# Kernel tuning notes

Measured on AMD Instinct MI355X. Metric: run time of the kernel, lower is better.

Reference implementation:

```python
import jax, jax.numpy as jnp
import numpy as np

B, T, I = 256, 2048, 128
H, L = 128, 2


def setup_inputs() -> dict:
    key = jax.random.key(0)
    ks = jax.random.split(key, 12)
    s_in = 1.0 / np.sqrt(I)
    s_h = 1.0 / np.sqrt(H)
    return {
        "x": jax.random.normal(ks[0], (B, T, I), jnp.float32),
        "Wz": jax.random.normal(ks[1], (L, I, H), jnp.float32) * s_in,
        "bz": jax.random.normal(ks[2], (L, H), jnp.float32) * s_in,
        "Uz": jax.random.normal(ks[3], (L, H, H), jnp.float32) * s_h,
        "Wr": jax.random.normal(ks[4], (L, I, H), jnp.float32) * s_in,
        "br": jax.random.normal(ks[5], (L, H), jnp.float32) * s_in,
        "Ur": jax.random.normal(ks[6], (L, H, H), jnp.float32) * s_h,
        "Wh": jax.random.normal(ks[7], (L, I, H), jnp.float32) * s_in,
        "bh": jax.random.normal(ks[8], (L, H), jnp.float32) * s_in,
        "Uh": jax.random.normal(ks[9], (L, H, H), jnp.float32) * s_h,
        "fc_w": jax.random.normal(ks[10], (H, 1), jnp.float32) * s_h,
        "fc_b": jax.random.normal(ks[11], (1,), jnp.float32) * s_h,
    }


def _gru_forward(x, Wz, bz, Uz, Wr, br, Ur, Wh, bh, Uh, fc_w, fc_b):
    nl = Wz.shape[0]
    batch = x.shape[0]
    hid = Uz.shape[-1]
    # Precompute layer-0 input projections for all timesteps: [T, B, H]
    pz0 = jnp.einsum('bti,ih->tbh', x, Wz[0]) + bz[0]
    pr0 = jnp.einsum('bti,ih->tbh', x, Wr[0]) + br[0]
    ph0 = jnp.einsum('bti,ih->tbh', x, Wh[0]) + bh[0]

    def step(h, proj_t):
        az0, ar0, ah0 = proj_t  # each [B, H]
        new_h = []
        prev = None
        for l in range(nl):
            if l == 0:
                az, ar, ah = az0, ar0, ah0
            else:
                az = prev @ Wz[l] + bz[l]
                ar = prev @ Wr[l] + br[l]
                ah = prev @ Wh[l] + bh[l]
            hl = h[l]
            z = jax.nn.sigmoid(az + hl @ Uz[l])
            r = jax.nn.sigmoid(ar + hl @ Ur[l])
            h_tilde = jnp.tanh(ah + (r * hl) @ Uh[l])
            hl = (1.0 - z) * hl + z * h_tilde
            new_h.append(hl)
            prev = hl
        return jnp.stack(new_h), None

    h0 = jnp.zeros((nl, batch, hid), x.dtype)
    h_final, _ = jax.lax.scan(step, h0, (pz0, pr0, ph0))
    return h_final[-1] @ fc_w + fc_b


def reference(x, Wz, bz, Uz, Wr, br, Ur, Wh, bh, Uh, fc_w, fc_b):
    return _gru_forward(x, Wz, bz, Uz, Wr, br, Ur, Wh, bh, Uh, fc_w, fc_b)
```

## Files before the change

kernel.cpp:

```cpp
#include <hip/hip_runtime.h>
#include <hip/hip_bf16.h>
#include <stdint.h>

#define T_STEPS 2048
#define BATCH   256
#define IDIM    128
#define HDIM    128

typedef __bf16 bf16x2 __attribute__((ext_vector_type(2)));

#if __has_builtin(__builtin_amdgcn_fdot2_f32_bf16)
#define HAVE_DOT2 1
#else
#define HAVE_DOT2 0
#endif

static __device__ __forceinline__ float d2(uint32_t a, uint32_t b, float c) {
#if HAVE_DOT2
  return __builtin_amdgcn_fdot2_f32_bf16(__builtin_bit_cast(bf16x2, a),
                                         __builtin_bit_cast(bf16x2, b), c, false);
#else
  float alo = __builtin_bit_cast(float, a << 16);
  float ahi = __builtin_bit_cast(float, a & 0xffff0000u);
  float blo = __builtin_bit_cast(float, b << 16);
  float bhi = __builtin_bit_cast(float, b & 0xffff0000u);
  return c + alo * blo + ahi * bhi;
#endif
}

static __device__ __forceinline__ uint32_t pack_bf16(float lo, float hi) {
  uint32_t a = (uint32_t)__builtin_bit_cast(unsigned short, __float2bfloat16(lo));
  uint32_t b = (uint32_t)__builtin_bit_cast(unsigned short, __float2bfloat16(hi));
  return a | (b << 16);
}

static __device__ __forceinline__ float sigmoidf_(float x) {
  return 1.f / (1.f + __expf(-x));
}
static __device__ __forceinline__ float tanhf_(float x) {
  return 1.f - 2.f / (1.f + __expf(2.f * x));
}

__global__ void pack_weights(const float* __restrict__ Wz, const float* __restrict__ Uz,
                             const float* __restrict__ Wr, const float* __restrict__ Ur,
                             const float* __restrict__ Wh, const float* __restrict__ Uh,
                             uint32_t* __restrict__ wpack) {
  int idx = blockIdx.x * blockDim.x + threadIdx.x;
  if (idx >= 12 * 4 * 128 * 16) return;
  int p = idx & 15;
  int j = (idx >> 4) & 127;
  int q = (idx >> 11) & 3;
  int m = idx >> 13;
  const float* src;
  switch (m) {
    case 0:  src = Wz;          break;
    case 1:  src = Wr;          break;
    case 2:  src = Wh;          break;
    case 3:  src = Uz;          break;
    case 4:  src = Ur;          break;
    case 5:  src = Uh;          break;
    case 6:  src = Uz + 16384;  break;
    case 7:  src = Ur + 16384;  break;
    case 8:  src = Wz + 16384;  break;
    case 9:  src = Wr + 16384;  break;
    case 10: src = Wh + 16384;  break;
    default: src = Uh + 16384;  break;
  }
  int i = q * 32 + p * 2;
  float lo = src[i * 128 + j];
  float hi = src[(i + 1) * 128 + j];
  wpack[idx] = pack_bf16(lo, hi);
}

#define QD(M)                                                          \
  {                                                                    \
    float a0 = 0.f, a1 = 0.f;                                          \
    a0 = d2(w[M][0].x, v0.x, a0); a0 = d2(w[M][0].y, v0.y, a0);        \
    a0 = d2(w[M][0].z, v0.z, a0); a0 = d2(w[M][0].w, v0.w, a0);        \
    a0 = d2(w[M][1].x, v1.x, a0); a0 = d2(w[M][1].y, v1.y, a0);        \
    a0 = d2(w[M][1].z, v1.z, a0); a0 = d2(w[M][1].w, v1.w, a0);        \
    a1 = d2(w[M][2].x, v2.x, a1); a1 = d2(w[M][2].y, v2.y, a1);        \
    a1 = d2(w[M][2].z, v2.z, a1); a1 = d2(w[M][2].w, v2.w, a1);        \
    a1 = d2(w[M][3].x, v3.x, a1); a1 = d2(w[M][3].y, v3.y, a1);        \
    a1 = d2(w[M][3].z, v3.z, a1); a1 = d2(w[M][3].w, v3.w, a1);        \
    part[(M * 4 + q) * 128 + j] = a0 + a1;                             \
  }

#define LOADV(VB)                                                      \
  const uint4* vp = (const uint4*)(VB);                                \
  uint4 v0 = vp[q * 4 + 0], v1 = vp[q * 4 + 1],                        \
        v2 = vp[q * 4 + 2], v3 = vp[q * 4 + 3];

#define PSUM(M)                                                        \
  ((part[(M * 4 + 0) * 128 + j2] + part[(M * 4 + 1) * 128 + j2]) +     \
   (part[(M * 4 + 2) * 128 + j2] + part[(M * 4 + 3) * 128 + j2]))

static __device__ __forceinline__ void pair_store(uint32_t* dst, int j2, float v) {
  uint32_t me = (uint32_t)__builtin_bit_cast(unsigned short, __float2bfloat16(v));
  uint32_t other = __shfl_xor((unsigned int)me, 1, 64);
  if ((j2 & 1) == 0) dst[j2 >> 1] = me | (other << 16);
}

__launch_bounds__(512, 2)
__global__ void gru_persist(const float* __restrict__ x,
                            const float* __restrict__ bz, const float* __restrict__ br,
                            const float* __restrict__ bh,
                            const float* __restrict__ fcw, const float* __restrict__ fcb,
                            const uint32_t* __restrict__ wpack,
                            float* __restrict__ out) {
  __shared__ float part[12 * 4 * 128];
  __shared__ float h0f[128], h1f[128], z0f[128], z1f[128];
  __shared__ uint32_t xbf[64], h0bf[64], h1bf[64], rh0bf[64], rh1bf[64];
  __shared__ float biasL[6 * 128];

  const int tid = threadIdx.x;
  const int j = tid & 127;
  const int q = tid >> 7;
  const int b = blockIdx.x;

  uint4 w[12][4];
  {
    const uint4* wp4 = (const uint4*)wpack;
#pragma unroll
    for (int m = 0; m < 12; ++m)
#pragma unroll
      for (int p = 0; p < 4; ++p)
        w[m][p] = wp4[((m * 4 + q) * 128 + j) * 4 + p];
  }

  if (tid < 128) {
    h0f[tid] = 0.f; h1f[tid] = 0.f;
    biasL[0 * 128 + tid] = bz[tid];
    biasL[1 * 128 + tid] = br[tid];
    biasL[2 * 128 + tid] = bh[tid];
    biasL[3 * 128 + tid] = bz[128 + tid];
    biasL[4 * 128 + tid] = br[128 + tid];
    biasL[5 * 128 + tid] = bh[128 + tid];
  }
  if (tid < 64) { h0bf[tid] = 0u; h1bf[tid] = 0u; }
  const float2* xrow = (const float2*)(x + (size_t)b * T_STEPS * IDIM);
  if (tid < 64) {
    float2 v = xrow[tid];
    xbf[tid] = pack_bf16(v.x, v.y);
  }
  __syncthreads();

  float2 xpre = make_float2(0.f, 0.f);
  for (int t = 0; t < T_STEPS; ++t) {
    if (tid < 64) {
      int tn = (t + 1 < T_STEPS) ? (t + 1) : t;
      xpre = xrow[tn * 64 + tid];
    }

    { LOADV(xbf);  QD(0); QD(1); QD(2); }
    { LOADV(h0bf); QD(3); QD(4); }
    { LOADV(h1bf); QD(6); QD(7); }
    __syncthreads();

    if (tid < 128) {
      const int j2 = tid;
      float az = biasL[0 * 128 + j2] + PSUM(0) + PSUM(3);
      float ar = biasL[1 * 128 + j2] + PSUM(1) + PSUM(4);
      float z = sigmoidf_(az);
      float r = sigmoidf_(ar);
      z0f[j2] = z;
      pair_store(rh0bf, j2, r * h0f[j2]);
    }
    __syncthreads();

    { LOADV(rh0bf); QD(5); }
    __syncthreads();

    if (tid < 128) {
      const int j2 = tid;
      float ah = biasL[2 * 128 + j2] + PSUM(2) + PSUM(5);
      float ht = tanhf_(ah);
      float z = z0f[j2];
      float hn = (1.f - z) * h0f[j2] + z * ht;
      h0f[j2] = hn;
      pair_store(h0bf, j2, hn);
    }
    __syncthreads();

    { LOADV(h0bf); QD(8); QD(9); QD(10); }
    __syncthreads();

    if (tid < 128) {
      const int j2 = tid;
      float az = biasL[3 * 128 + j2] + PSUM(8) + PSUM(6);
      float ar = biasL[4 * 128 + j2] + PSUM(9) + PSUM(7);
      float z = sigmoidf_(az);
      float r = sigmoidf_(ar);
      z1f[j2] = z;
      pair_store(rh1bf, j2, r * h1f[j2]);
    }
    __syncthreads();

    { LOADV(rh1bf); QD(11); }
    __syncthreads();

    if (tid < 128) {
      const int j2 = tid;
      float ah = biasL[5 * 128 + j2] + PSUM(10) + PSUM(11);
      float ht = tanhf_(ah);
      float z = z1f[j2];
      float hn = (1.f - z) * h1f[j2] + z * ht;
      h1f[j2] = hn;
      pair_store(h1bf, j2, hn);
    }
    if (tid < 64) xbf[tid] = pack_bf16(xpre.x, xpre.y);
    __syncthreads();
  }

  if (tid < 128) part[tid] = h1f[tid] * fcw[tid];
  __syncthreads();
  if (tid == 0) {
    float s = fcb[0];
#pragma unroll 8
    for (int i = 0; i < 128; ++i) s += part[i];
    out[b] = s;
  }
}

extern "C" void kernel_launch(void* const* d_in, const int* in_sizes, int n_in,
                              void* d_out, int out_size, void* d_ws, size_t ws_size,
                              hipStream_t stream) {
  const float* x   = (const float*)d_in[0];
  const float* Wz  = (const float*)d_in[1];
  const float* bz  = (const float*)d_in[2];
  const float* Uz  = (const float*)d_in[3];
  const float* Wr  = (const float*)d_in[4];
  const float* br  = (const float*)d_in[5];
  const float* Ur  = (const float*)d_in[6];
  const float* Wh  = (const float*)d_in[7];
  const float* bh  = (const float*)d_in[8];
  const float* Uh  = (const float*)d_in[9];
  const float* fcw = (const float*)d_in[10];
  const float* fcb = (const float*)d_in[11];
  uint32_t* wpack = (uint32_t*)d_ws;

  hipLaunchKernelGGL(pack_weights, dim3(384), dim3(256), 0, stream,
                     Wz, Uz, Wr, Ur, Wh, Uh, wpack);
  hipLaunchKernelGGL(gru_persist, dim3(BATCH), dim3(512), 0, stream,
                     x, bz, br, bh, fcw, fcb, wpack, (float*)d_out);
}
```

Baseline: 5.260 ms.

## Precompute layer-0 input projections in a separate kernel before the recurrent loop

Adds an xproj kernel that computes the layer-0 input projections (x·W plus bias) for all timesteps up front and stores them in workspace as fp32, or as bf16 when workspace is short. The persistent GRU kernel then streams these precomputed values instead of doing three 128x128 matvecs per step, so it holds 9 weight matrices in registers instead of 12. It also spreads the gate activations over 256 threads and pins the weight registers with empty asm. The cost is an extra kernel and a large workspace round-trip, about 800MB in fp32, with a fallback to the old path when workspace is too small.

```diff
diff --git a/kernel.cpp b/kernel.cpp
--- a/kernel.cpp
+++ b/kernel.cpp
@@ -33,12 +33,245 @@
   uint32_t b = (uint32_t)__builtin_bit_cast(unsigned short, __float2bfloat16(hi));
   return a | (b << 16);
 }
-
+static __device__ __forceinline__ unsigned short bf16bits(float v) {
+  return __builtin_bit_cast(unsigned short, __float2bfloat16(v));
+}
 static __device__ __forceinline__ float sigmoidf_(float x) {
   return 1.f / (1.f + __expf(-x));
 }
 static __device__ __forceinline__ float tanhf_(float x) {
   return 1.f - 2.f / (1.f + __expf(2.f * x));
+}
+
+#define NWU (9 * 4 * 128 * 16)
+#define NWP (384 * 64)
+
+__global__ void pack2(const float* __restrict__ Wz, const float* __restrict__ Uz,
+                      const float* __restrict__ Wr, const float* __restrict__ Ur,
+                      const float* __restrict__ Wh, const float* __restrict__ Uh,
+                      uint32_t* __restrict__ wpackU, uint32_t* __restrict__ wpackP) {
+  int idx = blockIdx.x * blockDim.x + threadIdx.x;
+  if (idx < NWU) {
+    int p = idx & 15;
+    int j = (idx >> 4) & 127;
+    int q = (idx >> 11) & 3;
+    int m = idx >> 13;
+    const float* src;
+    switch (m) {
+      case 0:  src = Uz;          break;
+      case 1:  src = Ur;          break;
+      case 2:  src = Uh;          break;
+      case 3:  src = Wz + 16384;  break;
+      case 4:  src = Wr + 16384;  break;
+      case 5:  src = Wh + 16384;  break;
+      case 6:  src = Uz + 16384;  break;
+      case 7:  src = Ur + 16384;  break;
+      default: src = Uh + 16384;  break;
+    }
+    int i = q * 32 + p * 2;
+    wpackU[idx] = pack_bf16(src[i * 128 + j], src[(i + 1) * 128 + j]);
+  } else if (idx < NWU + NWP) {
+    int k = idx - NWU;
+    int p = k & 63;
+    int c = k >> 6;
+    int g = c >> 7;
+    int j = c & 127;
+    const float* src = (g == 0) ? Wz : (g == 1) ? Wr : Wh;
+    wpackP[k] = pack_bf16(src[2 * p * 128 + j], src[(2 * p + 1) * 128 + j]);
+  }
+}
+
+template <int MODE>
+__global__ void xproj(const float* __restrict__ x,
+                      const float* __restrict__ bz, const float* __restrict__ br,
+                      const float* __restrict__ bh,
+                      const uint32_t* __restrict__ wpackP, void* __restrict__ proj) {
+  __shared__ uint32_t xs[64];
+  const int c = threadIdx.x;
+  const int g = c >> 7;
+  const int j = c & 127;
+  uint32_t wc[64];
+#pragma unroll
+  for (int p = 0; p < 64; ++p) wc[p] = wpackP[c * 64 + p];
+  const float bias = ((g == 0) ? bz : (g == 1) ? br : bh)[j];
+
+  const long r0 = (long)blockIdx.x * 512;
+  for (int rr = 0; rr < 512; ++rr) {
+    const long r = r0 + rr;
+    if (c < 64) {
+      float2 v = ((const float2*)(x + r * 128))[c];
+      xs[c] = pack_bf16(v.x, v.y);
+    }
+    __syncthreads();
+    float acc = bias;
+#pragma unroll
+    for (int p = 0; p < 64; ++p) acc = d2(wc[p], xs[p], acc);
+    if (MODE == 0)
+      ((float*)proj)[r * 384 + c] = acc;
+    else
+      ((unsigned short*)proj)[r * 384 + c] = bf16bits(acc);
+    __syncthreads();
+  }
+}
+
+#define QD(M)                                                          \
+  {                                                                    \
+    float a0 = 0.f, a1 = 0.f;                                          \
+    a0 = d2(w[M][0].x, v0.x, a0); a0 = d2(w[M][0].y, v0.y, a0);        \
+    a0 = d2(w[M][0].z, v0.z, a0); a0 = d2(w[M][0].w, v0.w, a0);        \
+    a0 = d2(w[M][1].x, v1.x, a0); a0 = d2(w[M][1].y, v1.y, a0);        \
+    a0 = d2(w[M][1].z, v1.z, a0); a0 = d2(w[M][1].w, v1.w, a0);        \
+    a1 = d2(w[M][2].x, v2.x, a1); a1 = d2(w[M][2].y, v2.y, a1);        \
+    a1 = d2(w[M][2].z, v2.z, a1); a1 = d2(w[M][2].w, v2.w, a1);        \
+    a1 = d2(w[M][3].x, v3.x, a1); a1 = d2(w[M][3].y, v3.y, a1);        \
+    a1 = d2(w[M][3].z, v3.z, a1); a1 = d2(w[M][3].w, v3.w, a1);        \
+    part[(M * 4 + q) * 128 + j] = a0 + a1;                             \
+  }
+
+#define LOADV(VB)                                                      \
+  const uint4* vp = (const uint4*)(VB);                                \
+  uint4 v0 = vp[q * 4 + 0], v1 = vp[q * 4 + 1],                        \
+        v2 = vp[q * 4 + 2], v3 = vp[q * 4 + 3];
+
+#define PSUM(M)                                                        \
+  ((part[(M * 4 + 0) * 128 + j2] + part[(M * 4 + 1) * 128 + j2]) +     \
+   (part[(M * 4 + 2) * 128 + j2] + part[(M * 4 + 3) * 128 + j2]))
+
+template <int MODE>
+__launch_bounds__(512, 2)
+__global__ void gru_persist2(const void* __restrict__ proj,
+                             const float* __restrict__ bz1, const float* __restrict__ br1,
+                             const float* __restrict__ bh1,
+                             const float* __restrict__ fcw, const float* __restrict__ fcb,
+                             const uint32_t* __restrict__ wpackU,
+                             float* __restrict__ out) {
+  __shared__ float part[9 * 4 * 128];
+  __shared__ float h0f[128], h1f[128], z0f[128];
+  __shared__ __align__(16) uint32_t h0bf[64], h1bf[64], rh0bf[64], rh1bf[64];
+  __shared__ float pbuf[384];
+  __shared__ float biasL[3 * 128];
+
+  const int tid = threadIdx.x;
+  const int j = tid & 127;
+  const int q = tid >> 7;
+  const int b = blockIdx.x;
+
+  uint4 w[9][4];
+  {
+    const uint4* wp4 = (const uint4*)wpackU;
+#pragma unroll
+    for (int m = 0; m < 9; ++m)
+#pragma unroll
+      for (int p = 0; p < 4; ++p)
+        w[m][p] = wp4[((m * 4 + q) * 128 + j) * 4 + p];
+  }
+#pragma unroll
+  for (int m = 0; m < 9; ++m)
+#pragma unroll
+    for (int p = 0; p < 4; ++p)
+      asm volatile("" : "+v"(w[m][p].x), "+v"(w[m][p].y),
+                        "+v"(w[m][p].z), "+v"(w[m][p].w));
+
+  if (tid < 128) {
+    h0f[tid] = 0.f; h1f[tid] = 0.f;
+    biasL[0 * 128 + tid] = bz1[tid];
+    biasL[1 * 128 + tid] = br1[tid];
+    biasL[2 * 128 + tid] = bh1[tid];
+  }
+  if (tid < 64) { h0bf[tid] = 0u; h1bf[tid] = 0u; }
+
+  const float*    prow32 = (const float*)proj + (size_t)b * T_STEPS * 384;
+  const uint32_t* prow16 = (const uint32_t*)proj + (size_t)b * T_STEPS * 192;
+  float    pc32 = 0.f;
+  uint32_t pc16 = 0u;
+  if (MODE == 0) { if (tid < 384) pc32 = prow32[tid]; }
+  else           { if (tid < 192) pc16 = prow16[tid]; }
+  __syncthreads();
+
+  for (int t = 0; t < T_STEPS; ++t) {
+    float pn32 = 0.f; uint32_t pn16 = 0u;
+    {
+      const int tn = (t + 1 < T_STEPS) ? (t + 1) : t;
+      if (MODE == 0) { if (tid < 384) pn32 = prow32[(size_t)tn * 384 + tid]; }
+      else           { if (tid < 192) pn16 = prow16[(size_t)tn * 192 + tid]; }
+    }
+
+    { LOADV(h0bf); QD(0); QD(1); }
+    { LOADV(h1bf); QD(6); QD(7); }
+    if (MODE == 0) {
+      if (tid < 384) pbuf[tid] = pc32;
+    } else {
+      if (tid < 192) {
+        pbuf[2 * tid]     = __builtin_bit_cast(float, pc16 << 16);
+        pbuf[2 * tid + 1] = __builtin_bit_cast(float, pc16 & 0xffff0000u);
+      }
+    }
+    __syncthreads();
+
+    if (tid < 256) {
+      const int j2 = tid & 127;
+      const bool isz = tid < 128;
+      const int M = isz ? 0 : 1;
+      float a = pbuf[(isz ? 0 : 128) + j2] + PSUM(M);
+      float gv = sigmoidf_(a);
+      if (isz) z0f[j2] = gv;
+      else     ((unsigned short*)rh0bf)[j2] = bf16bits(gv * h0f[j2]);
+    }
+    __syncthreads();
+
+    { LOADV(rh0bf); QD(2); }
+    __syncthreads();
+
+    if (tid < 128) {
+      const int j2 = tid;
+      float a = pbuf[256 + j2] + PSUM(2);
+      float ht = tanhf_(a);
+      float h = h0f[j2];
+      float hn = fmaf(z0f[j2], ht - h, h);
+      h0f[j2] = hn;
+      ((unsigned short*)h0bf)[j2] = bf16bits(hn);
+    }
+    __syncthreads();
+
+    { LOADV(h0bf); QD(3); QD(4); QD(5); }
+    __syncthreads();
+
+    if (tid < 256) {
+      const int j2 = tid & 127;
+      const bool isz = tid < 128;
+      float a = isz ? (biasL[j2]       + PSUM(3) + PSUM(6))
+                    : (biasL[128 + j2] + PSUM(4) + PSUM(7));
+      float gv = sigmoidf_(a);
+      if (isz) z0f[j2] = gv;
+      else     ((unsigned short*)rh1bf)[j2] = bf16bits(gv * h1f[j2]);
+    }
+    __syncthreads();
+
+    { LOADV(rh1bf); QD(8); }
+    __syncthreads();
+
+    if (tid < 128) {
+      const int j2 = tid;
+      float a = biasL[256 + j2] + PSUM(5) + PSUM(8);
+      float ht = tanhf_(a);
+      float h = h1f[j2];
+      float hn = fmaf(z0f[j2], ht - h, h);
+      h1f[j2] = hn;
+      ((unsigned short*)h1bf)[j2] = bf16bits(hn);
+    }
+    __syncthreads();
+
+    pc32 = pn32; pc16 = pn16;
+  }
+
+  if (tid < 128) part[tid] = h1f[tid] * fcw[tid];
+  __syncthreads();
+  if (tid == 0) {
+    float s = fcb[0];
+#pragma unroll 8
+    for (int i = 0; i < 128; ++i) s += part[i];
+    out[b] = s;
+  }
 }
 
 __global__ void pack_weights(const float* __restrict__ Wz, const float* __restrict__ Uz,
@@ -67,36 +300,11 @@
     default: src = Uh + 16384;  break;
   }
   int i = q * 32 + p * 2;
-  float lo = src[i * 128 + j];
-  float hi = src[(i + 1) * 128 + j];
-  wpack[idx] = pack_bf16(lo, hi);
-}
-
-#define QD(M)                                                          \
-  {                                                                    \
-    float a0 = 0.f, a1 = 0.f;                                          \
-    a0 = d2(w[M][0].x, v0.x, a0); a0 = d2(w[M][0].y, v0.y, a0);        \
-    a0 = d2(w[M][0].z, v0.z, a0); a0 = d2(w[M][0].w, v0.w, a0);        \
-    a0 = d2(w[M][1].x, v1.x, a0); a0 = d2(w[M][1].y, v1.y, a0);        \
-    a0 = d2(w[M][1].z, v1.z, a0); a0 = d2(w[M][1].w, v1.w, a0);        \
-    a1 = d2(w[M][2].x, v2.x, a1); a1 = d2(w[M][2].y, v2.y, a1);        \
-    a1 = d2(w[M][2].z, v2.z, a1); a1 = d2(w[M][2].w, v2.w, a1);        \
-    a1 = d2(w[M][3].x, v3.x, a1); a1 = d2(w[M][3].y, v3.y, a1);        \
-    a1 = d2(w[M][3].z, v3.z, a1); a1 = d2(w[M][3].w, v3.w, a1);        \
-    part[(M * 4 + q) * 128 + j] = a0 + a1;                             \
-  }
-
-#define LOADV(VB)                                                      \
-  const uint4* vp = (const uint4*)(VB);                                \
-  uint4 v0 = vp[q * 4 + 0], v1 = vp[q * 4 + 1],                        \
-        v2 = vp[q * 4 + 2], v3 = vp[q * 4 + 3];
-
-#define PSUM(M)                                                        \
-  ((part[(M * 4 + 0) * 128 + j2] + part[(M * 4 + 1) * 128 + j2]) +     \
-   (part[(M * 4 + 2) * 128 + j2] + part[(M * 4 + 3) * 128 + j2]))
+  wpack[idx] = pack_bf16(src[i * 128 + j], src[(i + 1) * 128 + j]);
+}
 
 static __device__ __forceinline__ void pair_store(uint32_t* dst, int j2, float v) {
-  uint32_t me = (uint32_t)__builtin_bit_cast(unsigned short, __float2bfloat16(v));
+  uint32_t me = (uint32_t)bf16bits(v);
   uint32_t other = __shfl_xor((unsigned int)me, 1, 64);
   if ((j2 & 1) == 0) dst[j2 >> 1] = me | (other << 16);
 }
@@ -110,7 +318,7 @@
                             float* __restrict__ out) {
   __shared__ float part[12 * 4 * 128];
   __shared__ float h0f[128], h1f[128], z0f[128], z1f[128];
-  __shared__ uint32_t xbf[64], h0bf[64], h1bf[64], rh0bf[64], rh1bf[64];
+  __shared__ __align__(16) uint32_t xbf[64], h0bf[64], h1bf[64], rh0bf[64], rh1bf[64];
   __shared__ float biasL[6 * 128];
 
   const int tid = threadIdx.x;
@@ -151,12 +359,10 @@
       int tn = (t + 1 < T_STEPS) ? (t + 1) : t;
       xpre = xrow[tn * 64 + tid];
     }
-
     { LOADV(xbf);  QD(0); QD(1); QD(2); }
     { LOADV(h0bf); QD(3); QD(4); }
     { LOADV(h1bf); QD(6); QD(7); }
     __syncthreads();
-
     if (tid < 128) {
       const int j2 = tid;
       float az = biasL[0 * 128 + j2] + PSUM(0) + PSUM(3);
@@ -167,10 +373,8 @@
       pair_store(rh0bf, j2, r * h0f[j2]);
     }
     __syncthreads();
-
     { LOADV(rh0bf); QD(5); }
     __syncthreads();
-
     if (tid < 128) {
       const int j2 = tid;
       float ah = biasL[2 * 128 + j2] + PSUM(2) + PSUM(5);
@@ -181,10 +385,8 @@
       pair_store(h0bf, j2, hn);
     }
     __syncthreads();
-
     { LOADV(h0bf); QD(8); QD(9); QD(10); }
     __syncthreads();
-
     if (tid < 128) {
       const int j2 = tid;
       float az = biasL[3 * 128 + j2] + PSUM(8) + PSUM(6);
@@ -195,10 +397,8 @@
       pair_store(rh1bf, j2, r * h1f[j2]);
     }
     __syncthreads();
-
     { LOADV(rh1bf); QD(11); }
     __syncthreads();
-
     if (tid < 128) {
       const int j2 = tid;
       float ah = biasL[5 * 128 + j2] + PSUM(10) + PSUM(11);
@@ -237,10 +437,38 @@
   const float* Uh  = (const float*)d_in[9];
   const float* fcw = (const float*)d_in[10];
   const float* fcb = (const float*)d_in[11];
-  uint32_t* wpack = (uint32_t*)d_ws;
-
-  hipLaunchKernelGGL(pack_weights, dim3(384), dim3(256), 0, stream,
-                     Wz, Uz, Wr, Ur, Wh, Uh, wpack);
-  hipLaunchKernelGGL(gru_persist, dim3(BATCH), dim3(512), 0, stream,
-                     x, bz, br, bh, fcw, fcb, wpack, (float*)d_out);
-}
+
+  const size_t R = (size_t)BATCH * T_STEPS;
+  const size_t bytesU = (size_t)NWU * 4;
+  const size_t bytesP = (size_t)NWP * 4;
+  const size_t projOff = bytesU + bytesP;
+  const size_t need32 = projOff + R * 384 * 4;
+  const size_t need16 = projOff + R * 384 * 2;
+
+  if (ws_size >= need16) {
+    uint32_t* wpackU = (uint32_t*)d_ws;
+    uint32_t* wpackP = (uint32_t*)((char*)d_ws + bytesU);
+    void* proj = (void*)((char*)d_ws + projOff);
+    hipLaunchKernelGGL(pack2, dim3((NWU + NWP) / 256), dim3(256), 0, stream,
+                       Wz, Uz, Wr, Ur, Wh, Uh, wpackU, wpackP);
+    if (ws_size >= need32) {
+      hipLaunchKernelGGL((xproj<0>), dim3(1024), dim3(384), 0, stream,
+                         x, bz, br, bh, wpackP, proj);
+      hipLaunchKernelGGL((gru_persist2<0>), dim3(BATCH), dim3(512), 0, stream,
+                         proj, bz + 128, br + 128, bh + 128, fcw, fcb, wpackU,
+                         (float*)d_out);
+    } else {
+      hipLaunchKernelGGL((xproj<1>), dim3(1024), dim3(384), 0, stream,
+                         x, bz, br, bh, wpackP, proj);
+      hipLaunchKernelGGL((gru_persist2<1>), dim3(BATCH), dim3(512), 0, stream,
+                         proj, bz + 128, br + 128, bh + 128, fcw, fcb, wpackU,
+                         (float*)d_out);
+    }
+  } else {
+    uint32_t* wpack = (uint32_t*)d_ws;
+    hipLaunchKernelGGL(pack_weights, dim3(384), dim3(256), 0, stream,
+                       Wz, Uz, Wr, Ur, Wh, Uh, wpack);
+    hipLaunchKernelGGL(gru_persist, dim3(BATCH), dim3(512), 0, stream,
+                       x, bz, br, bh, fcw, fcb, wpack, (float*)d_out);
+  }
+}
```

Result: faster. 5.057 ms (-3.9%).

## Precompute layer-0 input projections in a separate kernel; shorten recurrent critical path

Applied to the files above, without the earlier changes.

Adds a kernel that computes the layer-0 input projections (x·W + bias) for every timestep into workspace ahead of time. The recurrent kernel then only does the hidden-state matvecs, and they are split across 1024 threads (8 threads per output, combined with shuffle reductions). This cuts the serial per-step work and removes the shared-memory partial-sum passes and some barriers. The cost is a large projection buffer (about 800MB) written to and re-read from global memory. If the workspace is too small, the code falls back to the old path.

```diff
diff --git a/kernel.cpp b/kernel.cpp
--- a/kernel.cpp
+++ b/kernel.cpp
@@ -33,12 +33,230 @@
   uint32_t b = (uint32_t)__builtin_bit_cast(unsigned short, __float2bfloat16(hi));
   return a | (b << 16);
 }
-
+static __device__ __forceinline__ unsigned short bf16bits(float v) {
+  return __builtin_bit_cast(unsigned short, __float2bfloat16(v));
+}
 static __device__ __forceinline__ float sigmoidf_(float x) {
   return 1.f / (1.f + __expf(-x));
 }
 static __device__ __forceinline__ float tanhf_(float x) {
   return 1.f - 2.f / (1.f + __expf(2.f * x));
+}
+
+#define NWU (9 * 128 * 8 * 8)
+#define NWP (384 * 64)
+
+__global__ void pack3(const float* __restrict__ Wz, const float* __restrict__ Uz,
+                      const float* __restrict__ Wr, const float* __restrict__ Ur,
+                      const float* __restrict__ Wh, const float* __restrict__ Uh,
+                      uint32_t* __restrict__ wpackU, uint32_t* __restrict__ wpackP) {
+  int idx = blockIdx.x * blockDim.x + threadIdx.x;
+  if (idx < NWU) {
+    int p = idx & 7;
+    int o = (idx >> 3) & 7;
+    int jj = (idx >> 6) & 127;
+    int m = idx >> 13;
+    const float* src;
+    switch (m) {
+      case 0:  src = Uz;          break;
+      case 1:  src = Ur;          break;
+      case 2:  src = Uh;          break;
+      case 3:  src = Wz + 16384;  break;
+      case 4:  src = Wr + 16384;  break;
+      case 5:  src = Wh + 16384;  break;
+      case 6:  src = Uz + 16384;  break;
+      case 7:  src = Ur + 16384;  break;
+      default: src = Uh + 16384;  break;
+    }
+    int i = o * 16 + 2 * p;
+    wpackU[idx] = pack_bf16(src[i * 128 + jj], src[(i + 1) * 128 + jj]);
+  } else if (idx < NWU + NWP) {
+    int k = idx - NWU;
+    int p = k & 63;
+    int c = k >> 6;
+    int g = c >> 7;
+    int jj = c & 127;
+    const float* src = (g == 0) ? Wz : (g == 1) ? Wr : Wh;
+    wpackP[k] = pack_bf16(src[2 * p * 128 + jj], src[(2 * p + 1) * 128 + jj]);
+  }
+}
+
+__launch_bounds__(384)
+__global__ void xproj3(const float* __restrict__ x,
+                       const float* __restrict__ bz, const float* __restrict__ br,
+                       const float* __restrict__ bh,
+                       const uint32_t* __restrict__ wpackP, float* __restrict__ proj) {
+  __shared__ uint32_t xs[8][64];
+  const int tid = threadIdx.x;
+  const int g = tid >> 7;
+  const int j = tid & 127;
+  uint32_t wc[64];
+#pragma unroll
+  for (int p = 0; p < 64; ++p) wc[p] = wpackP[tid * 64 + p];
+  const float bias = ((g == 0) ? bz : (g == 1) ? br : bh)[j];
+
+  const long r0 = (long)blockIdx.x * 512;
+  for (int it = 0; it < 64; ++it) {
+    const long rbase = r0 + it * 8;
+    {
+      int ra = tid >> 6, ca = tid & 63;
+      float2 v = ((const float2*)(x + (rbase + ra) * 128))[ca];
+      xs[ra][ca] = pack_bf16(v.x, v.y);
+      if (tid < 128) {
+        int w2 = tid + 384;
+        int rb = w2 >> 6, cb = w2 & 63;
+        float2 v2 = ((const float2*)(x + (rbase + rb) * 128))[cb];
+        xs[rb][cb] = pack_bf16(v2.x, v2.y);
+      }
+    }
+    __syncthreads();
+    float acc[8];
+#pragma unroll
+    for (int rr = 0; rr < 8; ++rr) acc[rr] = bias;
+#pragma unroll 8
+    for (int p = 0; p < 64; ++p) {
+#pragma unroll
+      for (int rr = 0; rr < 8; ++rr) acc[rr] = d2(wc[p], xs[rr][p], acc[rr]);
+    }
+#pragma unroll
+    for (int rr = 0; rr < 8; ++rr) proj[(rbase + rr) * 384 + tid] = acc[rr];
+    __syncthreads();
+  }
+}
+
+#define QD8(M, ACC)                                                   \
+  {                                                                   \
+    float a0 = 0.f, a1 = 0.f;                                         \
+    a0 = d2(w[M][0].x, v0.x, a0); a0 = d2(w[M][0].y, v0.y, a0);       \
+    a0 = d2(w[M][0].z, v0.z, a0); a0 = d2(w[M][0].w, v0.w, a0);       \
+    a1 = d2(w[M][1].x, v1.x, a1); a1 = d2(w[M][1].y, v1.y, a1);       \
+    a1 = d2(w[M][1].z, v1.z, a1); a1 = d2(w[M][1].w, v1.w, a1);       \
+    ACC = a0 + a1;                                                    \
+  }
+
+#define RED3(A)                       \
+  A += __shfl_xor(A, 1, 64);          \
+  A += __shfl_xor(A, 2, 64);          \
+  A += __shfl_xor(A, 4, 64);
+
+#define PAIRW(DST, VAL)                                   \
+  {                                                       \
+    unsigned u = (unsigned)bf16bits(VAL);                 \
+    unsigned pu = __shfl_xor(u, 8, 64);                   \
+    if ((tid & 15) == 0) DST[j >> 1] = u | (pu << 16);    \
+  }
+
+__launch_bounds__(1024, 4)
+__global__ void gru3(const float* __restrict__ proj,
+                     const float* __restrict__ bz1, const float* __restrict__ br1,
+                     const float* __restrict__ bh1,
+                     const float* __restrict__ fcw, const float* __restrict__ fcb,
+                     const uint32_t* __restrict__ wpackU,
+                     float* __restrict__ out) {
+  __shared__ float pbuf[2][384];
+  __shared__ float h0f[128], h1f[128];
+  __shared__ __align__(16) uint32_t h0bf[64], h1bf[64], rh0bf[64], rh1bf[64];
+
+  const int tid = threadIdx.x;
+  const int j = tid >> 3;
+  const int o = tid & 7;
+  const int b = blockIdx.x;
+
+  uint4 w[9][2];
+  {
+    const uint4* wp4 = (const uint4*)wpackU;
+#pragma unroll
+    for (int m = 0; m < 9; ++m) {
+      w[m][0] = wp4[m * 2048 + tid * 2];
+      w[m][1] = wp4[m * 2048 + tid * 2 + 1];
+    }
+  }
+#pragma unroll
+  for (int m = 0; m < 9; ++m)
+    asm volatile("" : "+v"(w[m][0].x), "+v"(w[m][0].y), "+v"(w[m][0].z),
+                      "+v"(w[m][0].w), "+v"(w[m][1].x), "+v"(w[m][1].y),
+                      "+v"(w[m][1].z), "+v"(w[m][1].w));
+
+  const float bz1j = bz1[j];
+  const float br1j = br1[j];
+  const float bh1j = bh1[j];
+
+  const float* prow = proj + (size_t)b * T_STEPS * 384;
+
+  if (tid < 128) { h0f[tid] = 0.f; h1f[tid] = 0.f; }
+  if (tid < 64)  { h0bf[tid] = 0u; h1bf[tid] = 0u; }
+  if (tid < 384) pbuf[0][tid] = prow[tid];
+  __syncthreads();
+
+  for (int t = 0; t < T_STEPS; ++t) {
+    const int par = t & 1;
+    float pn = 0.f;
+    {
+      const int tn = (t + 1 < T_STEPS) ? (t + 1) : t;
+      if (tid < 384) pn = prow[(size_t)tn * 384 + tid];
+    }
+
+    float dz0, dr0, dz1, dr1;
+    {
+      uint4 v0 = ((const uint4*)h0bf)[2 * o], v1 = ((const uint4*)h0bf)[2 * o + 1];
+      QD8(0, dz0); QD8(1, dr0);
+    }
+    {
+      uint4 v0 = ((const uint4*)h1bf)[2 * o], v1 = ((const uint4*)h1bf)[2 * o + 1];
+      QD8(6, dz1); QD8(7, dr1);
+    }
+    RED3(dz0); RED3(dr0); RED3(dz1); RED3(dr1);
+    const float h0old = h0f[j];
+    const float z0 = sigmoidf_(pbuf[par][j] + dz0);
+    const float r0 = sigmoidf_(pbuf[par][128 + j] + dr0);
+    PAIRW(rh0bf, r0 * h0old);
+    __syncthreads();
+
+    float dh0;
+    {
+      uint4 v0 = ((const uint4*)rh0bf)[2 * o], v1 = ((const uint4*)rh0bf)[2 * o + 1];
+      QD8(2, dh0);
+    }
+    RED3(dh0);
+    const float ht0 = tanhf_(pbuf[par][256 + j] + dh0);
+    const float h0n = fmaf(z0, ht0 - h0old, h0old);
+    PAIRW(h0bf, h0n);
+    if (o == 0) h0f[j] = h0n;
+    __syncthreads();
+
+    float dwz1, dwr1, dwh1;
+    {
+      uint4 v0 = ((const uint4*)h0bf)[2 * o], v1 = ((const uint4*)h0bf)[2 * o + 1];
+      QD8(3, dwz1); QD8(4, dwr1); QD8(5, dwh1);
+    }
+    RED3(dwz1); RED3(dwr1); RED3(dwh1);
+    const float h1old = h1f[j];
+    const float z1 = sigmoidf_(bz1j + dwz1 + dz1);
+    const float r1 = sigmoidf_(br1j + dwr1 + dr1);
+    PAIRW(rh1bf, r1 * h1old);
+    if (tid < 384) pbuf[par ^ 1][tid] = pn;
+    __syncthreads();
+
+    float dh1;
+    {
+      uint4 v0 = ((const uint4*)rh1bf)[2 * o], v1 = ((const uint4*)rh1bf)[2 * o + 1];
+      QD8(8, dh1);
+    }
+    RED3(dh1);
+    const float ht1 = tanhf_(bh1j + dwh1 + dh1);
+    const float h1n = fmaf(z1, ht1 - h1old, h1old);
+    PAIRW(h1bf, h1n);
+    if (o == 0) h1f[j] = h1n;
+    __syncthreads();
+  }
+
+  if (tid < 64) {
+    float s = h1f[tid] * fcw[tid] + h1f[tid + 64] * fcw[tid + 64];
+    s += __shfl_xor(s, 32, 64); s += __shfl_xor(s, 16, 64);
+    s += __shfl_xor(s, 8, 64);  s += __shfl_xor(s, 4, 64);
+    s += __shfl_xor(s, 2, 64);  s += __shfl_xor(s, 1, 64);
+    if (tid == 0) out[b] = s + fcb[0];
+  }
 }
 
 __global__ void pack_weights(const float* __restrict__ Wz, const float* __restrict__ Uz,
@@ -67,9 +285,7 @@
     default: src = Uh + 16384;  break;
   }
   int i = q * 32 + p * 2;
-  float lo = src[i * 128 + j];
-  float hi = src[(i + 1) * 128 + j];
-  wpack[idx] = pack_bf16(lo, hi);
+  wpack[idx] = pack_bf16(src[i * 128 + j], src[(i + 1) * 128 + j]);
 }
 
 #define QD(M)                                                          \
@@ -96,7 +312,7 @@
    (part[(M * 4 + 2) * 128 + j2] + part[(M * 4 + 3) * 128 + j2]))
 
 static __device__ __forceinline__ void pair_store(uint32_t* dst, int j2, float v) {
-  uint32_t me = (uint32_t)__builtin_bit_cast(unsigned short, __float2bfloat16(v));
+  uint32_t me = (uint32_t)bf16bits(v);
   uint32_t other = __shfl_xor((unsigned int)me, 1, 64);
   if ((j2 & 1) == 0) dst[j2 >> 1] = me | (other << 16);
 }
@@ -110,7 +326,7 @@
                             float* __restrict__ out) {
   __shared__ float part[12 * 4 * 128];
   __shared__ float h0f[128], h1f[128], z0f[128], z1f[128];
-  __shared__ uint32_t xbf[64], h0bf[64], h1bf[64], rh0bf[64], rh1bf[64];
+  __shared__ __align__(16) uint32_t xbf[64], h0bf[64], h1bf[64], rh0bf[64], rh1bf[64];
   __shared__ float biasL[6 * 128];
 
   const int tid = threadIdx.x;
@@ -151,12 +367,10 @@
       int tn = (t + 1 < T_STEPS) ? (t + 1) : t;
       xpre = xrow[tn * 64 + tid];
     }
-
     { LOADV(xbf);  QD(0); QD(1); QD(2); }
     { LOADV(h0bf); QD(3); QD(4); }
     { LOADV(h1bf); QD(6); QD(7); }
     __syncthreads();
-
     if (tid < 128) {
       const int j2 = tid;
       float az = biasL[0 * 128 + j2] + PSUM(0) + PSUM(3);
@@ -167,10 +381,8 @@
       pair_store(rh0bf, j2, r * h0f[j2]);
     }
     __syncthreads();
-
     { LOADV(rh0bf); QD(5); }
     __syncthreads();
-
     if (tid < 128) {
       const int j2 = tid;
       float ah = biasL[2 * 128 + j2] + PSUM(2) + PSUM(5);
@@ -181,10 +393,8 @@
       pair_store(h0bf, j2, hn);
     }
     __syncthreads();
-
     { LOADV(h0bf); QD(8); QD(9); QD(10); }
     __syncthreads();
-
     if (tid < 128) {
       const int j2 = tid;
       float az = biasL[3 * 128 + j2] + PSUM(8) + PSUM(6);
@@ -195,10 +405,8 @@
       pair_store(rh1bf, j2, r * h1f[j2]);
     }
     __syncthreads();
-
     { LOADV(rh1bf); QD(11); }
     __syncthreads();
-
     if (tid < 128) {
       const int j2 = tid;
       float ah = biasL[5 * 128 + j2] + PSUM(10) + PSUM(11);
@@ -237,10 +445,29 @@
   const float* Uh  = (const float*)d_in[9];
   const float* fcw = (const float*)d_in[10];
   const float* fcb = (const float*)d_in[11];
-  uint32_t* wpack = (uint32_t*)d_ws;
-
-  hipLaunchKernelGGL(pack_weights, dim3(384), dim3(256), 0, stream,
-                     Wz, Uz, Wr, Ur, Wh, Uh, wpack);
-  hipLaunchKernelGGL(gru_persist, dim3(BATCH), dim3(512), 0, stream,
-                     x, bz, br, bh, fcw, fcb, wpack, (float*)d_out);
-}
+
+  const size_t R = (size_t)BATCH * T_STEPS;
+  const size_t bytesU = (size_t)NWU * 4;
+  const size_t bytesP = (size_t)NWP * 4;
+  const size_t projOff = bytesU + bytesP;
+  const size_t need32 = projOff + R * 384 * 4;
+
+  if (ws_size >= need32) {
+    uint32_t* wpackU = (uint32_t*)d_ws;
+    uint32_t* wpackP = (uint32_t*)((char*)d_ws + bytesU);
+    float* proj = (float*)((char*)d_ws + projOff);
+    hipLaunchKernelGGL(pack3, dim3((NWU + NWP + 255) / 256), dim3(256), 0, stream,
+                       Wz, Uz, Wr, Ur, Wh, Uh, wpackU, wpackP);
+    hipLaunchKernelGGL(xproj3, dim3(1024), dim3(384), 0, stream,
+                       x, bz, br, bh, wpackP, proj);
+    hipLaunchKernelGGL(gru3, dim3(BATCH), dim3(1024), 0, stream,
+                       proj, bz + 128, br + 128, bh + 128, fcw, fcb, wpackU,
+                       (float*)d_out);
+  } else {
+    uint32_t* wpack = (uint32_t*)d_ws;
+    hipLaunchKernelGGL(pack_weights, dim3(384), dim3(256), 0, stream,
+                       Wz, Uz, Wr, Ur, Wh, Uh, wpack);
+    hipLaunchKernelGGL(gru_persist, dim3(BATCH), dim3(512), 0, stream,
+                       x, bz, br, bh, fcw, fcb, wpack, (float*)d_out);
+  }
+}
```

Measured after the change: 6.787 ms. +29.0%, slower.
